# Kernel optimization log

Hardware: AMD Instinct MI355X
Metric: run time of the kernel (lower is better)

## Reference

```python
import jax, jax.numpy as jnp
import numpy as np

B, K, N, D, L, H = 32768, 10, 200000, 128, 100, 512


def setup_inputs() -> dict:
    key = jax.random.key(0)
    ks = jax.random.split(key, 10)
    return {
        "nodes": jax.random.randint(ks[0], (B,), 0, N),
        "neighs": jax.random.randint(ks[1], (B, K), 0, N),
        "embed": jax.random.normal(ks[2], (N, D), dtype=jnp.float32),
        "feature_labels": jax.random.randint(ks[3], (N,), 0, L),
        "distance": jax.random.uniform(ks[4], (L, L), dtype=jnp.float32),
        "spectral_vec": jax.random.uniform(ks[5], (N,), dtype=jnp.float32),
        "freq": jax.random.uniform(ks[6], (B, K), dtype=jnp.float32),
        "dist_e": jax.random.uniform(ks[7], (B, K), dtype=jnp.float32),
        "W1": jax.random.normal(ks[8], (H, 4), dtype=jnp.float32) * (6.0 / (H + 4)) ** 0.5,
        "b1": jnp.zeros((H,), dtype=jnp.float32),
        "W2": jax.random.normal(ks[9], (H,), dtype=jnp.float32) * (6.0 / (H + 1)) ** 0.5,
        "b2": jnp.zeros((1,), dtype=jnp.float32),
    }


def reference(nodes, neighs, embed, feature_labels, distance, spectral_vec,
              freq, dist_e, W1, b1, W2, b2):
    k = neighs.shape[1]
    lab_i = feature_labels[nodes]                 # [B]
    lab_j = feature_labels[neighs]                # [B,K]
    dist_cs = distance[lab_i[:, None], lab_j]     # [B,K]
    spec = spectral_vec[neighs]                   # [B,K]
    # per-edge 4-dim summary, as in get_imp
    s = jnp.stack([freq, dist_e, dist_cs, spec], axis=-1)        # [B,K,4]
    h = jax.nn.sigmoid(jnp.einsum('bkf,hf->bkh', s, W1) + b1)    # [B,K,H]
    imp = jax.nn.sigmoid(jnp.einsum('bkh,h->bk', h, W2) + b2[0])  # [B,K]
    # mask = 1/num_neigh per sampled neighbor, multiplied by importance
    w = imp / jnp.float32(k)                                      # [B,K]
    return jnp.einsum('bk,bkd->bd', w, embed[neighs])             # [B,D]
```

## Files before the change

kernel.cpp:

```cpp
#include <hip/hip_runtime.h>
#include <hip/hip_bf16.h>

#define B_SZ 32768
#define K_SZ 10
#define N_SZ 200000
#define D_SZ 128
#define L_SZ 100
#define H_SZ 512

typedef float v2f __attribute__((ext_vector_type(2)));

__global__ __launch_bounds__(256) void agg_kernel(
    const int*   __restrict__ nodes,
    const int*   __restrict__ neighs,
    const float* __restrict__ embed,
    const int*   __restrict__ labels,
    const float* __restrict__ distance,
    const float* __restrict__ spectral,
    const float* __restrict__ freq,
    const float* __restrict__ dist_e,
    const float* __restrict__ W1,
    const float* __restrict__ b1,
    const float* __restrict__ W2,
    const float* __restrict__ b2,
    float*       __restrict__ out)
{
    const int lane = threadIdx.x & 63;
    const int b = __builtin_amdgcn_readfirstlane(
        (blockIdx.x * 256 + (int)threadIdx.x) >> 6);

    int nb[K_SZ];
#pragma unroll
    for (int k = 0; k < K_SZ; ++k) nb[k] = neighs[b * K_SZ + k];

    v2f e[K_SZ];
#pragma unroll
    for (int k = 0; k < K_SZ; ++k)
        e[k] = ((const v2f*)(embed + (size_t)nb[k] * D_SZ))[lane];

    float4 w1r[8];
    float  b1r[8], w2r[8];
#pragma unroll
    for (int i = 0; i < 8; ++i) {
        const int h = lane + 64 * i;
        w1r[i] = ((const float4*)W1)[h];
        b1r[i] = b1[h];
        w2r[i] = W2[h];
    }
    float w2s[4];
#pragma unroll
    for (int j = 0; j < 4; ++j) w2s[j] = w2r[2*j] + w2r[2*j+1];
    const float b2v = b2[0];

    const int   node  = nodes[b];
    const int   lab_i = labels[node];
    const float* __restrict__ distRow = distance + (size_t)lab_i * L_SZ;

    float f0[K_SZ], f1[K_SZ], f2[K_SZ], f3[K_SZ];
#pragma unroll
    for (int k = 0; k < K_SZ; ++k) {
        f0[k] = freq[b * K_SZ + k];
        f1[k] = dist_e[b * K_SZ + k];
    }
    int labj[K_SZ];
#pragma unroll
    for (int k = 0; k < K_SZ; ++k) labj[k] = labels[nb[k]];
#pragma unroll
    for (int k = 0; k < K_SZ; ++k) {
        f2[k] = distRow[labj[k]];
        f3[k] = spectral[nb[k]];
    }

    float part[K_SZ];
#pragma unroll
    for (int k = 0; k < K_SZ; ++k) {
        float p = 0.f;
#pragma unroll
        for (int j = 0; j < 4; ++j) {
            const float4 wa = w1r[2*j], wb = w1r[2*j+1];
            const float xa = fmaf(wa.x, f0[k], fmaf(wa.y, f1[k],
                             fmaf(wa.z, f2[k], fmaf(wa.w, f3[k], b1r[2*j]))));
            const float xb = fmaf(wb.x, f0[k], fmaf(wb.y, f1[k],
                             fmaf(wb.z, f2[k], fmaf(wb.w, f3[k], b1r[2*j+1]))));
            const float ua = __expf(-xa);
            const float ub = __expf(-xb);
            const float num = fmaf(w2r[2*j], ub, fmaf(w2r[2*j+1], ua, w2s[j]));
            const float den = fmaf(ua, ub, (1.f + ua) + ub);
            p = fmaf(num, __builtin_amdgcn_rcpf(den), p);
        }
        part[k] = p;
    }

#pragma unroll
    for (int off = 32; off > 0; off >>= 1) {
#pragma unroll
        for (int k = 0; k < K_SZ; ++k)
            part[k] += __shfl_xor(part[k], off, 64);
    }

    float acc0 = 0.f, acc1 = 0.f;
#pragma unroll
    for (int k = 0; k < K_SZ; ++k) {
        const float imp = __builtin_amdgcn_rcpf(1.f + __expf(-(part[k] + b2v)));
        const float w   = imp * 0.1f;
        acc0 = fmaf(w, e[k].x, acc0);
        acc1 = fmaf(w, e[k].y, acc1);
    }

    v2f r; r.x = acc0; r.y = acc1;
    __builtin_nontemporal_store(r, (v2f*)(out + (size_t)b * D_SZ) + lane);
}

extern "C" void kernel_launch(void* const* d_in, const int* in_sizes, int n_in,
                              void* d_out, int out_size, void* d_ws, size_t ws_size,
                              hipStream_t stream) {
    const int*   nodes    = (const int*)  d_in[0];
    const int*   neighs   = (const int*)  d_in[1];
    const float* embed    = (const float*)d_in[2];
    const int*   labels   = (const int*)  d_in[3];
    const float* distance = (const float*)d_in[4];
    const float* spectral = (const float*)d_in[5];
    const float* freq     = (const float*)d_in[6];
    const float* dist_e   = (const float*)d_in[7];
    const float* W1       = (const float*)d_in[8];
    const float* b1       = (const float*)d_in[9];
    const float* W2       = (const float*)d_in[10];
    const float* b2       = (const float*)d_in[11];
    float* out = (float*)d_out;

    const int threads = 256;
    const int blocks  = (B_SZ * 64) / threads;
    agg_kernel<<<blocks, threads, 0, stream>>>(
        nodes, neighs, embed, labels, distance, spectral,
        freq, dist_e, W1, b1, W2, b2, out);
}
```

Measured before the change: 214.7 us.

## Split into per-edge MLP kernel and separate vectorized gather kernel

```diff
diff --git a/kernel.cpp b/kernel.cpp
--- a/kernel.cpp
+++ b/kernel.cpp
@@ -1,19 +1,17 @@
 #include <hip/hip_runtime.h>
-#include <hip/hip_bf16.h>
 
 #define B_SZ 32768
 #define K_SZ 10
-#define N_SZ 200000
+#define NK   (B_SZ * K_SZ)
 #define D_SZ 128
 #define L_SZ 100
 #define H_SZ 512
 
-typedef float v2f __attribute__((ext_vector_type(2)));
+typedef float v4f __attribute__((ext_vector_type(4)));
 
-__global__ __launch_bounds__(256) void agg_kernel(
+__global__ __launch_bounds__(256) void mlp_kernel(
     const int*   __restrict__ nodes,
     const int*   __restrict__ neighs,
-    const float* __restrict__ embed,
     const int*   __restrict__ labels,
     const float* __restrict__ distance,
     const float* __restrict__ spectral,
@@ -23,92 +21,66 @@
     const float* __restrict__ b1,
     const float* __restrict__ W2,
     const float* __restrict__ b2,
+    float*       __restrict__ wout)
+{
+    const unsigned id = blockIdx.x * 256u + threadIdx.x;
+    const unsigned b  = id / 10u;
+
+    const int   nb = neighs[id];
+    const float f0 = freq[id];
+    const float f1 = dist_e[id];
+    const int   li = labels[nodes[b]];
+    const float f2 = distance[li * L_SZ + labels[nb]];
+    const float f3 = spectral[nb];
+
+    float acc = 0.f;
+#pragma unroll 4
+    for (int p = 0; p < H_SZ / 2; ++p) {
+        const int ha = 2 * p, hb = 2 * p + 1;
+        const float xa = fmaf(W1[4*ha+0], f0, fmaf(W1[4*ha+1], f1,
+                         fmaf(W1[4*ha+2], f2, W1[4*ha+3] * f3))) + b1[ha];
+        const float xb = fmaf(W1[4*hb+0], f0, fmaf(W1[4*hb+1], f1,
+                         fmaf(W1[4*hb+2], f2, W1[4*hb+3] * f3))) + b1[hb];
+        const float ua = __expf(-xa), ub = __expf(-xb);
+        const float ta = 1.f + ua,    tb = 1.f + ub;
+        const float num = fmaf(W2[ha], tb, W2[hb] * ta);
+        const float den = ta * tb;
+        acc = fmaf(num, __builtin_amdgcn_rcpf(den), acc);
+    }
+    const float imp = __builtin_amdgcn_rcpf(1.f + __expf(-(acc + b2[0])));
+    wout[id] = imp * 0.1f;
+}
+
+__global__ __launch_bounds__(256) void gather_kernel(
+    const int*   __restrict__ neighs,
+    const float* __restrict__ embed,
+    const float* __restrict__ w,
     float*       __restrict__ out)
 {
+    const int tid  = blockIdx.x * 256 + (int)threadIdx.x;
+    const int wv   = __builtin_amdgcn_readfirstlane(tid >> 6);
     const int lane = threadIdx.x & 63;
-    const int b = __builtin_amdgcn_readfirstlane(
-        (blockIdx.x * 256 + (int)threadIdx.x) >> 6);
+    const int half = lane >> 5;
+    const int l    = lane & 31;
+    const int bA = wv * 2, bB = wv * 2 + 1;
 
-    int nb[K_SZ];
-#pragma unroll
-    for (int k = 0; k < K_SZ; ++k) nb[k] = neighs[b * K_SZ + k];
-
-    v2f e[K_SZ];
-#pragma unroll
-    for (int k = 0; k < K_SZ; ++k)
-        e[k] = ((const v2f*)(embed + (size_t)nb[k] * D_SZ))[lane];
-
-    float4 w1r[8];
-    float  b1r[8], w2r[8];
-#pragma unroll
-    for (int i = 0; i < 8; ++i) {
-        const int h = lane + 64 * i;
-        w1r[i] = ((const float4*)W1)[h];
-        b1r[i] = b1[h];
-        w2r[i] = W2[h];
-    }
-    float w2s[4];
-#pragma unroll
-    for (int j = 0; j < 4; ++j) w2s[j] = w2r[2*j] + w2r[2*j+1];
-    const float b2v = b2[0];
-
-    const int   node  = nodes[b];
-    const int   lab_i = labels[node];
-    const float* __restrict__ distRow = distance + (size_t)lab_i * L_SZ;
-
-    float f0[K_SZ], f1[K_SZ], f2[K_SZ], f3[K_SZ];
+    v4f a = {0.f, 0.f, 0.f, 0.f};
 #pragma unroll
     for (int k = 0; k < K_SZ; ++k) {
-        f0[k] = freq[b * K_SZ + k];
-        f1[k] = dist_e[b * K_SZ + k];
+        const int   n0 = neighs[bA * K_SZ + k];
+        const int   n1 = neighs[bB * K_SZ + k];
+        const float w0 = w[bA * K_SZ + k];
+        const float w1 = w[bB * K_SZ + k];
+        const int   n  = half ? n1 : n0;
+        const float ww = half ? w1 : w0;
+        const v4f   e  = ((const v4f*)(embed + (size_t)n * D_SZ))[l];
+        a.x = fmaf(ww, e.x, a.x);
+        a.y = fmaf(ww, e.y, a.y);
+        a.z = fmaf(ww, e.z, a.z);
+        a.w = fmaf(ww, e.w, a.w);
     }
-    int labj[K_SZ];
-#pragma unroll
-    for (int k = 0; k < K_SZ; ++k) labj[k] = labels[nb[k]];
-#pragma unroll
-    for (int k = 0; k < K_SZ; ++k) {
-        f2[k] = distRow[labj[k]];
-        f3[k] = spectral[nb[k]];
-    }
-
-    float part[K_SZ];
-#pragma unroll
-    for (int k = 0; k < K_SZ; ++k) {
-        float p = 0.f;
-#pragma unroll
-        for (int j = 0; j < 4; ++j) {
-            const float4 wa = w1r[2*j], wb = w1r[2*j+1];
-            const float xa = fmaf(wa.x, f0[k], fmaf(wa.y, f1[k],
-                             fmaf(wa.z, f2[k], fmaf(wa.w, f3[k], b1r[2*j]))));
-            const float xb = fmaf(wb.x, f0[k], fmaf(wb.y, f1[k],
-                             fmaf(wb.z, f2[k], fmaf(wb.w, f3[k], b1r[2*j+1]))));
-            const float ua = __expf(-xa);
-            const float ub = __expf(-xb);
-            const float num = fmaf(w2r[2*j], ub, fmaf(w2r[2*j+1], ua, w2s[j]));
-            const float den = fmaf(ua, ub, (1.f + ua) + ub);
-            p = fmaf(num, __builtin_amdgcn_rcpf(den), p);
-        }
-        part[k] = p;
-    }
-
-#pragma unroll
-    for (int off = 32; off > 0; off >>= 1) {
-#pragma unroll
-        for (int k = 0; k < K_SZ; ++k)
-            part[k] += __shfl_xor(part[k], off, 64);
-    }
-
-    float acc0 = 0.f, acc1 = 0.f;
-#pragma unroll
-    for (int k = 0; k < K_SZ; ++k) {
-        const float imp = __builtin_amdgcn_rcpf(1.f + __expf(-(part[k] + b2v)));
-        const float w   = imp * 0.1f;
-        acc0 = fmaf(w, e[k].x, acc0);
-        acc1 = fmaf(w, e[k].y, acc1);
-    }
-
-    v2f r; r.x = acc0; r.y = acc1;
-    __builtin_nontemporal_store(r, (v2f*)(out + (size_t)b * D_SZ) + lane);
+    const int b = half ? bB : bA;
+    __builtin_nontemporal_store(a, (v4f*)(out + (size_t)b * D_SZ) + l);
 }
 
 extern "C" void kernel_launch(void* const* d_in, const int* in_sizes, int n_in,
@@ -126,11 +98,13 @@
     const float* b1       = (const float*)d_in[9];
     const float* W2       = (const float*)d_in[10];
     const float* b2       = (const float*)d_in[11];
-    float* out = (float*)d_out;
+    float* out  = (float*)d_out;
+    float* wbuf = (float*)d_ws;
 
-    const int threads = 256;
-    const int blocks  = (B_SZ * 64) / threads;
-    agg_kernel<<<blocks, threads, 0, stream>>>(
-        nodes, neighs, embed, labels, distance, spectral,
-        freq, dist_e, W1, b1, W2, b2, out);
+    mlp_kernel<<<NK / 256, 256, 0, stream>>>(
+        nodes, neighs, labels, distance, spectral,
+        freq, dist_e, W1, b1, W2, b2, wbuf);
+
+    gather_kernel<<<(B_SZ / 2 * 64) / 256, 256, 0, stream>>>(
+        neighs, embed, wbuf, out);
 }
```

Result: slower. 237.6 us (+10.6%).

## Process four batch rows per wave and fold the log2e scale into the weights

Applied to the files above, without the earlier changes.

```diff
diff --git a/kernel.cpp b/kernel.cpp
--- a/kernel.cpp
+++ b/kernel.cpp
@@ -1,16 +1,22 @@
 #include <hip/hip_runtime.h>
-#include <hip/hip_bf16.h>
 
 #define B_SZ 32768
 #define K_SZ 10
-#define N_SZ 200000
 #define D_SZ 128
 #define L_SZ 100
-#define H_SZ 512
+#define BPW  4
 
 typedef float v2f __attribute__((ext_vector_type(2)));
+typedef float v4f __attribute__((ext_vector_type(4)));
 
-__global__ __launch_bounds__(256) void agg_kernel(
+#if __has_builtin(__builtin_amdgcn_exp2f)
+#define EXP2(x) __builtin_amdgcn_exp2f(x)
+#else
+#define EXP2(x) __expf((x) * 0.69314718055994531f)
+#endif
+#define RCP(x) __builtin_amdgcn_rcpf(x)
+
+__global__ __launch_bounds__(256) void agg_fused(
     const int*   __restrict__ nodes,
     const int*   __restrict__ neighs,
     const float* __restrict__ embed,
@@ -26,89 +32,90 @@
     float*       __restrict__ out)
 {
     const int lane = threadIdx.x & 63;
-    const int b = __builtin_amdgcn_readfirstlane(
+    const int wv = __builtin_amdgcn_readfirstlane(
         (blockIdx.x * 256 + (int)threadIdx.x) >> 6);
 
-    int nb[K_SZ];
-#pragma unroll
-    for (int k = 0; k < K_SZ; ++k) nb[k] = neighs[b * K_SZ + k];
-
-    v2f e[K_SZ];
-#pragma unroll
-    for (int k = 0; k < K_SZ; ++k)
-        e[k] = ((const v2f*)(embed + (size_t)nb[k] * D_SZ))[lane];
-
-    float4 w1r[8];
-    float  b1r[8], w2r[8];
+    const float NL2E = -1.44269504088896f;
+    v4f   w1s[8];
+    float b1s[8], w2r[8];
 #pragma unroll
     for (int i = 0; i < 8; ++i) {
         const int h = lane + 64 * i;
-        w1r[i] = ((const float4*)W1)[h];
-        b1r[i] = b1[h];
+        w1s[i] = ((const v4f*)W1)[h] * NL2E;
+        b1s[i] = b1[h] * NL2E;
         w2r[i] = W2[h];
     }
-    float w2s[4];
 #pragma unroll
-    for (int j = 0; j < 4; ++j) w2s[j] = w2r[2*j] + w2r[2*j+1];
-    const float b2v = b2[0];
+    for (int i = 0; i < 8; ++i)
+        asm volatile("" : "+v"(w1s[i]), "+v"(b1s[i]), "+v"(w2r[i]));
+    const float b2s = b2[0] * NL2E;
 
-    const int   node  = nodes[b];
-    const int   lab_i = labels[node];
-    const float* __restrict__ distRow = distance + (size_t)lab_i * L_SZ;
+    for (int bi = 0; bi < BPW; ++bi) {
+        const int b = wv * BPW + bi;
 
-    float f0[K_SZ], f1[K_SZ], f2[K_SZ], f3[K_SZ];
+        int nb[K_SZ];
 #pragma unroll
-    for (int k = 0; k < K_SZ; ++k) {
-        f0[k] = freq[b * K_SZ + k];
-        f1[k] = dist_e[b * K_SZ + k];
-    }
-    int labj[K_SZ];
+        for (int k = 0; k < K_SZ; ++k) nb[k] = neighs[b * K_SZ + k];
+
+        v2f e[K_SZ];
 #pragma unroll
-    for (int k = 0; k < K_SZ; ++k) labj[k] = labels[nb[k]];
+        for (int k = 0; k < K_SZ; ++k)
+            e[k] = ((const v2f*)(embed + (size_t)nb[k] * D_SZ))[lane];
+
+        const int li = labels[nodes[b]];
+        const float* __restrict__ distRow = distance + li * L_SZ;
+        float f0[K_SZ], f1[K_SZ], f2[K_SZ], f3[K_SZ];
 #pragma unroll
-    for (int k = 0; k < K_SZ; ++k) {
-        f2[k] = distRow[labj[k]];
-        f3[k] = spectral[nb[k]];
-    }
+        for (int k = 0; k < K_SZ; ++k) {
+            f0[k] = freq[b * K_SZ + k];
+            f1[k] = dist_e[b * K_SZ + k];
+        }
+        int labj[K_SZ];
+#pragma unroll
+        for (int k = 0; k < K_SZ; ++k) labj[k] = labels[nb[k]];
+#pragma unroll
+        for (int k = 0; k < K_SZ; ++k) {
+            f2[k] = distRow[labj[k]];
+            f3[k] = spectral[nb[k]];
+        }
 
-    float part[K_SZ];
+        float part[K_SZ];
 #pragma unroll
-    for (int k = 0; k < K_SZ; ++k) {
-        float p = 0.f;
+        for (int k = 0; k < K_SZ; ++k) {
+            float p = 0.f;
 #pragma unroll
-        for (int j = 0; j < 4; ++j) {
-            const float4 wa = w1r[2*j], wb = w1r[2*j+1];
-            const float xa = fmaf(wa.x, f0[k], fmaf(wa.y, f1[k],
-                             fmaf(wa.z, f2[k], fmaf(wa.w, f3[k], b1r[2*j]))));
-            const float xb = fmaf(wb.x, f0[k], fmaf(wb.y, f1[k],
-                             fmaf(wb.z, f2[k], fmaf(wb.w, f3[k], b1r[2*j+1]))));
-            const float ua = __expf(-xa);
-            const float ub = __expf(-xb);
-            const float num = fmaf(w2r[2*j], ub, fmaf(w2r[2*j+1], ua, w2s[j]));
-            const float den = fmaf(ua, ub, (1.f + ua) + ub);
-            p = fmaf(num, __builtin_amdgcn_rcpf(den), p);
+            for (int j = 0; j < 4; ++j) {
+                const v4f   wa = w1s[2*j],   wb = w1s[2*j+1];
+                const float xa = fmaf(wa.x, f0[k], fmaf(wa.y, f1[k],
+                                 fmaf(wa.z, f2[k], fmaf(wa.w, f3[k], b1s[2*j]))));
+                const float xb = fmaf(wb.x, f0[k], fmaf(wb.y, f1[k],
+                                 fmaf(wb.z, f2[k], fmaf(wb.w, f3[k], b1s[2*j+1]))));
+                const float ua = EXP2(xa), ub = EXP2(xb);
+                const float ta = 1.f + ua,  tb = 1.f + ub;
+                const float num = fmaf(w2r[2*j], tb, w2r[2*j+1] * ta);
+                p = fmaf(num, RCP(ta * tb), p);
+            }
+            part[k] = p;
         }
-        part[k] = p;
-    }
 
 #pragma unroll
-    for (int off = 32; off > 0; off >>= 1) {
+        for (int off = 32; off > 0; off >>= 1) {
 #pragma unroll
-        for (int k = 0; k < K_SZ; ++k)
-            part[k] += __shfl_xor(part[k], off, 64);
+            for (int k = 0; k < K_SZ; ++k)
+                part[k] += __shfl_xor(part[k], off, 64);
+        }
+
+        float acc0 = 0.f, acc1 = 0.f;
+#pragma unroll
+        for (int k = 0; k < K_SZ; ++k) {
+            const float imp = RCP(1.f + EXP2(fmaf(part[k], NL2E, b2s)));
+            const float w   = imp * 0.1f;
+            acc0 = fmaf(w, e[k].x, acc0);
+            acc1 = fmaf(w, e[k].y, acc1);
+        }
+        v2f r; r.x = acc0; r.y = acc1;
+        __builtin_nontemporal_store(r, (v2f*)(out + (size_t)b * D_SZ) + lane);
     }
-
-    float acc0 = 0.f, acc1 = 0.f;
-#pragma unroll
-    for (int k = 0; k < K_SZ; ++k) {
-        const float imp = __builtin_amdgcn_rcpf(1.f + __expf(-(part[k] + b2v)));
-        const float w   = imp * 0.1f;
-        acc0 = fmaf(w, e[k].x, acc0);
-        acc1 = fmaf(w, e[k].y, acc1);
-    }
-
-    v2f r; r.x = acc0; r.y = acc1;
-    __builtin_nontemporal_store(r, (v2f*)(out + (size_t)b * D_SZ) + lane);
 }
 
 extern "C" void kernel_launch(void* const* d_in, const int* in_sizes, int n_in,
@@ -128,9 +135,7 @@
     const float* b2       = (const float*)d_in[11];
     float* out = (float*)d_out;
 
-    const int threads = 256;
-    const int blocks  = (B_SZ * 64) / threads;
-    agg_kernel<<<blocks, threads, 0, stream>>>(
+    agg_fused<<<(B_SZ / BPW * 64) / 256, 256, 0, stream>>>(
         nodes, neighs, embed, labels, distance, spectral,
         freq, dist_e, W1, b1, W2, b2, out);
 }
```

New measurement: 227.1 us. 1.06x slower.
